# Kernel tuning notes

Hardware: AMD Instinct MI355X
Metric: run time of the kernel (lower is better)

The kernel has to match this reference:

```python
import jax, jax.numpy as jnp
import numpy as np
import math

N = 4096
D = 256


def _xavier(key, shape):
    fan_in, fan_out = shape[0], shape[1]
    std = math.sqrt(2.0 / (fan_in + fan_out))
    return jax.random.normal(key, shape, dtype=jnp.float32) * std


def setup_inputs() -> dict:
    key = jax.random.key(0)
    ks = jax.random.split(key, 12)
    return {
        "cur": jax.random.normal(ks[0], (N, D), dtype=jnp.float32),
        "pre": jax.random.normal(ks[1], (N, D), dtype=jnp.float32),
        # SpatialHyperedge params
        "r_proj_s": _xavier(ks[2], (D, D)),
        "incidence_s": _xavier(ks[3], (N, N - 1)),
        # TemporalHyperedge params
        "r_proj_t": _xavier(ks[4], (D, D)),
        "incidence_t": _xavier(ks[5], (N, N)),
        # HHNodeMP params
        "node_proj": _xavier(ks[6], (D, D)),
        "spa_edge_proj": _xavier(ks[7], (D, D)),
        "tmp_edge_proj": _xavier(ks[8], (D, D)),
        "theta_w": _xavier(ks[9], (D, D)),
        "theta_b": jnp.zeros((D,), dtype=jnp.float32),
    }


def _scatter_slave(vals):
    """Place [N, N-1] per-row slave values into a zero-diagonal [N, N] matrix.
    Row i's k-th slave is column k if k < i else k+1 (all j != i in order)."""
    n = vals.shape[0]
    k = jnp.arange(n - 1)[None, :]
    cols = k + (k >= jnp.arange(n)[:, None])  # [N, N-1] column indices
    rows = jnp.broadcast_to(jnp.arange(n)[:, None], (n, n - 1))
    return jnp.zeros((n, n), dtype=vals.dtype).at[rows.reshape(-1), cols.reshape(-1)].set(vals.reshape(-1))


def _fro(x):
    return jnp.sqrt(jnp.sum(x * x))


def reference(cur, pre, r_proj_s, incidence_s, r_proj_t, incidence_t,
              node_proj, spa_edge_proj, tmp_edge_proj, theta_w, theta_b):
    n, d = cur.shape
    inv_sqrt_d = 1.0 / math.sqrt(d)

    # ---- SpatialHyperedge ----
    Xd = jax.lax.stop_gradient(cur)
    master_s = Xd @ r_proj_s                                   # [N, D]
    M_s_full = _scatter_slave(incidence_s)                     # [N, N], zero diag
    neigh_recon_s = M_s_full @ Xd                              # == bmm over gathered slaves
    spatial_loss = (_fro(master_s - neigh_recon_s) * 0.2
                    + jnp.sum(jnp.abs(incidence_s))
                    + 0.001 * _fro(incidence_s))
    # clamp(min=0) then zero-out entries not strictly > 0  => relu-like
    clipped_s = jnp.where(incidence_s > 0.0, incidence_s, 0.0)
    incidence_all = _scatter_slave(clipped_s) + jnp.eye(n, dtype=cur.dtype)

    # ---- TemporalHyperedge ----
    cur_d = jax.lax.stop_gradient(cur)
    pre_d = jax.lax.stop_gradient(pre)
    master_t = cur_d @ r_proj_t
    neigh_recon_t = incidence_t @ pre_d
    temporal_loss = (_fro(master_t - neigh_recon_t) * 0.2
                     + jnp.sum(jnp.abs(incidence_t))
                     + 0.001 * _fro(incidence_t))
    incidence_t_clipped = jnp.maximum(incidence_t, 0.0)

    # ---- SpatialHyperedgeMP ----
    spa_edge_fea = incidence_all @ cur
    spa_deg = jnp.sum(incidence_all, axis=1, keepdims=True)
    spa_emb = spa_edge_fea / spa_deg                           # [N, D]

    # ---- TemporalHyperedgeMP ----
    tmp_edge_fea = incidence_t_clipped @ pre + cur
    tmp_deg = jnp.sum(incidence_t_clipped, axis=1, keepdims=True) + 1.0
    tmp_emb = tmp_edge_fea / tmp_deg                           # [N, D]

    # ---- HHNodeMP ----
    node_fea = cur @ node_proj
    spa_fea = spa_emb @ spa_edge_proj
    tmp_fea = tmp_emb @ tmp_edge_proj
    spa_attn = jnp.sum(spa_fea * node_fea, axis=1, keepdims=True) * inv_sqrt_d
    tmp_attn = jnp.sum(tmp_fea * node_fea, axis=1, keepdims=True) * inv_sqrt_d
    val = spa_attn * spa_fea + tmp_attn * tmp_fea
    node_emb = jax.nn.relu(val @ theta_w.T + theta_b)          # dropout = identity (eval)

    return node_emb, temporal_loss + spatial_loss
```

## Files before the change

kernel.cpp:

```cpp
#include <hip/hip_runtime.h>
#include <hip/hip_bf16.h>
#include <math.h>

#define NN 4096
#define DD 256

typedef __bf16 bf16x8 __attribute__((ext_vector_type(8)));
typedef short  short8 __attribute__((ext_vector_type(8)));
typedef float  f32x4  __attribute__((ext_vector_type(4)));

#define MFMA16(a, b, c) __builtin_amdgcn_mfma_f32_16x16x32_bf16((a), (b), (c), 0, 0, 0)

__device__ inline bf16x8 brelu(bf16x8 a) {
    short8 s = __builtin_bit_cast(short8, a);
    s = s & ~(s >> 15);
    return __builtin_bit_cast(bf16x8, s);
}

__device__ inline float wave_red(float v) {
#pragma unroll
    for (int o = 32; o > 0; o >>= 1) v += __shfl_down(v, o, 64);
    return v;
}

__device__ inline unsigned short bfbits(float f) {
    return __builtin_bit_cast(unsigned short, (__bf16)f);
}

__global__ __launch_bounds__(256) void k_prep(const float* __restrict__ cur,
                                              const float* __restrict__ pre,
                                              __bf16* __restrict__ cur_bf,
                                              __bf16* __restrict__ curT,
                                              __bf16* __restrict__ preT) {
    const int z = blockIdx.z;
    const int i0 = blockIdx.x * 64, d0 = blockIdx.y * 64;
    const float* src = z ? pre : cur;
    __bf16* dstT = z ? preT : curT;
    __shared__ unsigned short tile[64][72];
    const int t = threadIdx.x;
    const int r = t >> 2, c4 = (t & 3) * 16;
    const float* srow = src + (size_t)(i0 + r) * DD + d0 + c4;
    alignas(16) unsigned short loc[16];
#pragma unroll
    for (int e = 0; e < 4; ++e) {
        float4 v = ((const float4*)srow)[e];
        loc[e * 4 + 0] = bfbits(v.x);
        loc[e * 4 + 1] = bfbits(v.y);
        loc[e * 4 + 2] = bfbits(v.z);
        loc[e * 4 + 3] = bfbits(v.w);
    }
#pragma unroll
    for (int e = 0; e < 16; ++e) tile[r][c4 + e] = loc[e];
    if (z == 0) {
        __bf16* drow = cur_bf + (size_t)(i0 + r) * DD + d0 + c4;
        *(uint4*)drow = *(uint4*)&loc[0];
        *(uint4*)(drow + 8) = *(uint4*)&loc[8];
    }
    __syncthreads();
    alignas(16) unsigned short o[16];
#pragma unroll
    for (int e = 0; e < 16; ++e) o[e] = tile[c4 + e][r];
    __bf16* trow = dstT + (size_t)(d0 + r) * NN + i0 + c4;
    *(uint4*)trow = *(uint4*)&o[0];
    *(uint4*)(trow + 8) = *(uint4*)&o[8];
}

__global__ __launch_bounds__(256) void k_proj(
    const float* __restrict__ a0, const float* __restrict__ a1, const float* __restrict__ a2,
    const float* __restrict__ a3, const float* __restrict__ a4, const float* __restrict__ a5,
    __bf16* __restrict__ o0, __bf16* __restrict__ o1, __bf16* __restrict__ o2,
    __bf16* __restrict__ o3, __bf16* __restrict__ o4, __bf16* __restrict__ o5) {
    const int id = blockIdx.y, r = blockIdx.x, t = threadIdx.x;
    const float* src = id == 0 ? a0 : id == 1 ? a1 : id == 2 ? a2 : id == 3 ? a3 : id == 4 ? a4 : a5;
    __bf16* dst = id == 0 ? o0 : id == 1 ? o1 : id == 2 ? o2 : id == 3 ? o3 : id == 4 ? o4 : o5;
    float v = src[r * DD + t];
    if (id < 5) dst[t * DD + r] = (__bf16)v;
    else        dst[r * DD + t] = (__bf16)v;
}

__global__ __launch_bounds__(256) void k_conv(const float* __restrict__ incT, const float* __restrict__ incS,
                                              __bf16* __restrict__ Mt, __bf16* __restrict__ Ms,
                                              float* __restrict__ rsT, float* __restrict__ rsS,
                                              float* __restrict__ pAbsT, float* __restrict__ pSqT,
                                              float* __restrict__ pAbsS, float* __restrict__ pSqS) {
    const int i = blockIdx.x, t = threadIdx.x;
    __shared__ unsigned short row[NN];
    __shared__ float red[3][4];
    float rs = 0.f, as = 0.f, qs = 0.f;
    if (blockIdx.y == 0) {
        const float4* src = (const float4*)(incT + (size_t)i * NN);
        ushort4* dst = (ushort4*)(Mt + (size_t)i * NN);
#pragma unroll
        for (int e = 0; e < 4; ++e) {
            const int f = t + 256 * e;
            float4 v = src[f];
            float x[4] = {v.x, v.y, v.z, v.w};
            unsigned short o[4];
#pragma unroll
            for (int j = 0; j < 4; ++j) {
                float fv = x[j];
                as += fabsf(fv); qs += fv * fv; rs += fmaxf(fv, 0.f);
                o[j] = bfbits(fv);
            }
            dst[f] = make_ushort4(o[0], o[1], o[2], o[3]);
        }
        const int w = t >> 6, lane = t & 63;
        rs = wave_red(rs); as = wave_red(as); qs = wave_red(qs);
        if (lane == 0) { red[0][w] = rs; red[1][w] = as; red[2][w] = qs; }
        __syncthreads();
        if (t == 0) {
            rsT[i]   = red[0][0] + red[0][1] + red[0][2] + red[0][3];
            pAbsT[i] = red[1][0] + red[1][1] + red[1][2] + red[1][3];
            pSqT[i]  = red[2][0] + red[2][1] + red[2][2] + red[2][3];
        }
    } else {
        const float* srow = incS + (size_t)i * (NN - 1);
#pragma unroll
        for (int e = 0; e < 4; ++e) {
            const int f = t + 256 * e;
            float x[4] = {0.f, 0.f, 0.f, 0.f};
            if (f < 1023) __builtin_memcpy(x, srow + 4 * f, 16);
            else          __builtin_memcpy(x, srow + 4092, 12);
#pragma unroll
            for (int j = 0; j < 4; ++j) {
                const int k = 4 * f + j;
                float fv = x[j];
                as += fabsf(fv); qs += fv * fv; rs += fmaxf(fv, 0.f);
                if (k < NN - 1) row[k + (k >= i)] = bfbits(fv);
            }
        }
        if (t == 0) row[i] = 0;
        __syncthreads();
        uint4* dOut = (uint4*)(Ms + (size_t)i * NN);
        const uint4* sIn = (const uint4*)row;
        dOut[t] = sIn[t];
        dOut[t + 256] = sIn[t + 256];
        const int w = t >> 6, lane = t & 63;
        rs = wave_red(rs); as = wave_red(as); qs = wave_red(qs);
        if (lane == 0) { red[0][w] = rs; red[1][w] = as; red[2][w] = qs; }
        __syncthreads();
        if (t == 0) {
            rsS[i]   = red[0][0] + red[0][1] + red[0][2] + red[0][3];
            pAbsS[i] = red[1][0] + red[1][1] + red[1][2] + red[1][3];
            pSqS[i]  = red[2][0] + red[2][1] + red[2][2] + red[2][3];
        }
    }
}

__global__ __launch_bounds__(256) void k_big(const __bf16* __restrict__ Mt, const __bf16* __restrict__ Ms,
                                             const __bf16* __restrict__ preT, const __bf16* __restrict__ curT,
                                             const float* __restrict__ negMt, const float* __restrict__ negMs,
                                             const float* __restrict__ cur,
                                             float* __restrict__ feaT, float* __restrict__ feaS,
                                             float* __restrict__ pDiff) {
    const int z = blockIdx.y;
    const __bf16* A  = z ? Ms : Mt;
    const __bf16* BT = z ? curT : preT;
    const float* negM = z ? negMs : negMt;
    float* fea = z ? feaS : feaT;
    const int m0 = blockIdx.x * 32;
    __shared__ __bf16 As[2][32][64];
    __shared__ float sred[4];
    const int t = threadIdx.x, w = t >> 6, lane = t & 63, quad = lane >> 4, l16 = lane & 15;
    const int rsw = l16 & 7;
    const int srow = t >> 3, sc8 = t & 7;
    const int swz = (sc8 ^ (srow & 7)) * 8;
    const __bf16* gA = A + (size_t)(m0 + srow) * NN + sc8 * 8;
    const int nb = w * 64;
    const __bf16* gB[4];
#pragma unroll
    for (int nf = 0; nf < 4; ++nf)
        gB[nf] = BT + (size_t)(nb + nf * 16 + l16) * NN + quad * 8;

    f32x4 accR[2][4], accL[2][4];
#pragma unroll
    for (int mi = 0; mi < 2; ++mi)
#pragma unroll
        for (int nf = 0; nf < 4; ++nf) { accR[mi][nf] = (f32x4)0.f; accL[mi][nf] = (f32x4)0.f; }

    bf16x8 b[2][2][4];
    uint4 preA;
    {
        uint4 a0 = *(const uint4*)gA; gA += 64;
        *(uint4*)&As[0][srow][swz] = a0;
        preA = *(const uint4*)gA; gA += 64;
#pragma unroll
        for (int ks = 0; ks < 2; ++ks)
#pragma unroll
            for (int nf = 0; nf < 4; ++nf)
                b[0][ks][nf] = *(const bf16x8*)(gB[nf] + ks * 32);
        __syncthreads();
    }
#pragma unroll 2
    for (int kt = 0; kt < 64; ++kt) {
        const int cb = kt & 1;
        if (kt < 63) *(uint4*)&As[cb ^ 1][srow][swz] = preA;
        if (kt < 62) { preA = *(const uint4*)gA; gA += 64; }
        if (kt < 63) {
#pragma unroll
            for (int ks = 0; ks < 2; ++ks)
#pragma unroll
                for (int nf = 0; nf < 4; ++nf)
                    b[cb ^ 1][ks][nf] = *(const bf16x8*)(gB[nf] + (kt + 1) * 64 + ks * 32);
        }
        bf16x8 a[2][2];
#pragma unroll
        for (int ks = 0; ks < 2; ++ks) {
            const int col = ((ks * 4 + quad) ^ rsw) * 8;
#pragma unroll
            for (int mi = 0; mi < 2; ++mi)
                a[ks][mi] = *(const bf16x8*)&As[cb][mi * 16 + l16][col];
        }
#pragma unroll
        for (int ks = 0; ks < 2; ++ks)
#pragma unroll
            for (int mi = 0; mi < 2; ++mi) {
                bf16x8 ar = brelu(a[ks][mi]);
#pragma unroll
                for (int nf = 0; nf < 4; ++nf) {
                    accR[mi][nf] = MFMA16(a[ks][mi], b[cb][ks][nf], accR[mi][nf]);
                    accL[mi][nf] = MFMA16(ar, b[cb][ks][nf], accL[mi][nf]);
                }
            }
        __syncthreads();
    }
    float sumd = 0.f;
#pragma unroll
    for (int mi = 0; mi < 2; ++mi)
#pragma unroll
        for (int nf = 0; nf < 4; ++nf)
#pragma unroll
            for (int r = 0; r < 4; ++r) {
                int gr = m0 + mi * 16 + quad * 4 + r;
                int gc = nb + nf * 16 + l16;
                size_t idx = (size_t)gr * DD + gc;
                float diff = accR[mi][nf][r] + negM[idx];
                sumd += diff * diff;
                fea[idx] = accL[mi][nf][r] + cur[idx];
            }
    sumd = wave_red(sumd);
    if (lane == 0) sred[w] = sumd;
    __syncthreads();
    if (t == 0) pDiff[z * 128 + blockIdx.x] = sred[0] + sred[1] + sred[2] + sred[3];
}

template <int DUAL>
__device__ inline void mfma_step(const __bf16 (&As)[64][72], const __bf16 (&Bs)[64][72],
                                 int wr, int wc, int quad, int l16,
                                 f32x4 (&accR)[2][2], f32x4 (&accL)[2][2]) {
#pragma unroll
    for (int ks = 0; ks < 2; ++ks) {
        const int kc = ks * 32 + quad * 8;
        bf16x8 a0 = *(const bf16x8*)&As[wr * 32 + l16][kc];
        bf16x8 a1 = *(const bf16x8*)&As[wr * 32 + 16 + l16][kc];
        bf16x8 b0 = *(const bf16x8*)&Bs[wc * 32 + l16][kc];
        bf16x8 b1 = *(const bf16x8*)&Bs[wc * 32 + 16 + l16][kc];
        accR[0][0] = MFMA16(a0, b0, accR[0][0]);
        accR[0][1] = MFMA16(a0, b1, accR[0][1]);
        accR[1][0] = MFMA16(a1, b0, accR[1][0]);
        accR[1][1] = MFMA16(a1, b1, accR[1][1]);
        if (DUAL) {
            bf16x8 a0r = brelu(a0), a1r = brelu(a1);
            accL[0][0] = MFMA16(a0r, b0, accL[0][0]);
            accL[0][1] = MFMA16(a0r, b1, accL[0][1]);
            accL[1][0] = MFMA16(a1r, b0, accL[1][0]);
            accL[1][1] = MFMA16(a1r, b1, accL[1][1]);
        }
    }
}

__global__ __launch_bounds__(256) void k_small3(const __bf16* __restrict__ cur_bf,
                                                const __bf16* __restrict__ pTs, const __bf16* __restrict__ pTt,
                                                const __bf16* __restrict__ pTn,
                                                float* __restrict__ negMs, float* __restrict__ negMt,
                                                float* __restrict__ nodeFea) {
    const int z = blockIdx.z;
    const __bf16* BT = z == 0 ? pTs : (z == 1 ? pTt : pTn);
    const int n0 = blockIdx.x * 64, m0 = blockIdx.y * 64;
    __shared__ __bf16 As[64][72], Bs[64][72];
    f32x4 accR[2][2];
#pragma unroll
    for (int i = 0; i < 2; ++i)
#pragma unroll
        for (int j = 0; j < 2; ++j) accR[i][j] = (f32x4)0.f;
    const int t = threadIdx.x, w = t >> 6, lane = t & 63, quad = lane >> 4, l16 = lane & 15;
    const int wr = w >> 1, wc = w & 1;
    const int sr = t >> 2, sc = (t & 3) * 16;
    const __bf16* gA = cur_bf + (size_t)(m0 + sr) * DD + sc;
    const __bf16* gB = BT + (size_t)(n0 + sr) * DD + sc;
    for (int kt = 0; kt < DD / 64; ++kt) {
        uint4 av0 = *(const uint4*)(gA);
        uint4 av1 = *(const uint4*)(gA + 8);
        uint4 bv0 = *(const uint4*)(gB);
        uint4 bv1 = *(const uint4*)(gB + 8);
        __syncthreads();
        *(uint4*)&As[sr][sc] = av0; *(uint4*)&As[sr][sc + 8] = av1;
        *(uint4*)&Bs[sr][sc] = bv0; *(uint4*)&Bs[sr][sc + 8] = bv1;
        __syncthreads();
        mfma_step<0>(As, Bs, wr, wc, quad, l16, accR, accR);
        gA += 64; gB += 64;
    }
#pragma unroll
    for (int mi = 0; mi < 2; ++mi)
#pragma unroll
        for (int ni = 0; ni < 2; ++ni)
#pragma unroll
            for (int r = 0; r < 4; ++r) {
                int gr = m0 + wr * 32 + mi * 16 + quad * 4 + r;
                int gc = n0 + wc * 32 + ni * 16 + l16;
                size_t idx = (size_t)gr * DD + gc;
                float v = accR[mi][ni][r];
                if (z == 0) negMs[idx] = -v;
                else if (z == 1) negMt[idx] = -v;
                else nodeFea[idx] = v;
            }
}

__global__ __launch_bounds__(256) void k_fea(const float* __restrict__ feaS, const float* __restrict__ feaT,
                                             const float* __restrict__ rsS, const float* __restrict__ rsT,
                                             const __bf16* __restrict__ pTspa, const __bf16* __restrict__ pTtmp,
                                             float* __restrict__ spaF, float* __restrict__ tmpF) {
    const int z = blockIdx.z;
    const float* fea = z ? feaT : feaS;
    const float* rs = z ? rsT : rsS;
    const __bf16* BT = z ? pTtmp : pTspa;
    float* outF = z ? tmpF : spaF;
    const int n0 = blockIdx.x * 64, m0 = blockIdx.y * 64;
    __shared__ __bf16 As[64][72], Bs[64][72];
    f32x4 accR[2][2];
#pragma unroll
    for (int i = 0; i < 2; ++i)
#pragma unroll
        for (int j = 0; j < 2; ++j) accR[i][j] = (f32x4)0.f;
    const int t = threadIdx.x, w = t >> 6, lane = t & 63, quad = lane >> 4, l16 = lane & 15;
    const int wr = w >> 1, wc = w & 1;
    const int sr = t >> 2, sc = (t & 3) * 16;
    const float inv = 1.f / (rs[m0 + sr] + 1.f);
    const float* gA = fea + (size_t)(m0 + sr) * DD + sc;
    const __bf16* gB = BT + (size_t)(n0 + sr) * DD + sc;
    for (int kt = 0; kt < DD / 64; ++kt) {
        __bf16 tmp[16];
#pragma unroll
        for (int e4 = 0; e4 < 4; ++e4) {
            float4 v = ((const float4*)gA)[e4];
            tmp[e4 * 4 + 0] = (__bf16)(v.x * inv);
            tmp[e4 * 4 + 1] = (__bf16)(v.y * inv);
            tmp[e4 * 4 + 2] = (__bf16)(v.z * inv);
            tmp[e4 * 4 + 3] = (__bf16)(v.w * inv);
        }
        uint4 bv0 = *(const uint4*)(gB);
        uint4 bv1 = *(const uint4*)(gB + 8);
        __syncthreads();
        *(uint4*)&As[sr][sc] = *(uint4*)&tmp[0]; *(uint4*)&As[sr][sc + 8] = *(uint4*)&tmp[8];
        *(uint4*)&Bs[sr][sc] = bv0; *(uint4*)&Bs[sr][sc + 8] = bv1;
        __syncthreads();
        mfma_step<0>(As, Bs, wr, wc, quad, l16, accR, accR);
        gA += 64; gB += 64;
    }
#pragma unroll
    for (int mi = 0; mi < 2; ++mi)
#pragma unroll
        for (int ni = 0; ni < 2; ++ni)
#pragma unroll
            for (int r = 0; r < 4; ++r) {
                int gr = m0 + wr * 32 + mi * 16 + quad * 4 + r;
                int gc = n0 + wc * 32 + ni * 16 + l16;
                outF[(size_t)gr * DD + gc] = accR[mi][ni][r];
            }
}

__global__ __launch_bounds__(256) void k_attn(const float* __restrict__ spaF, const float* __restrict__ tmpF,
                                              const float* __restrict__ nodeF,
                                              float* __restrict__ spaA, float* __restrict__ tmpA) {
    const int t = threadIdx.x, w = t >> 6, lane = t & 63;
    const int i = blockIdx.x * 4 + w;
    const float4* sf = (const float4*)(spaF + (size_t)i * DD);
    const float4* tf = (const float4*)(tmpF + (size_t)i * DD);
    const float4* nf = (const float4*)(nodeF + (size_t)i * DD);
    float4 s = sf[lane], p = tf[lane], n = nf[lane];
    float ds = s.x * n.x + s.y * n.y + s.z * n.z + s.w * n.w;
    float dt = p.x * n.x + p.y * n.y + p.z * n.z + p.w * n.w;
    ds = wave_red(ds); dt = wave_red(dt);
    if (lane == 0) { spaA[i] = ds * 0.0625f; tmpA[i] = dt * 0.0625f; }
}

__global__ __launch_bounds__(256) void k_final(const float* __restrict__ spaF, const float* __restrict__ tmpF,
                                               const float* __restrict__ spaA, const float* __restrict__ tmpA,
                                               const __bf16* __restrict__ thetaBf, const float* __restrict__ thetaB,
                                               float* __restrict__ out) {
    const int n0 = blockIdx.x * 64, m0 = blockIdx.y * 64;
    __shared__ __bf16 As[64][72], Bs[64][72];
    f32x4 accR[2][2];
#pragma unroll
    for (int i = 0; i < 2; ++i)
#pragma unroll
        for (int j = 0; j < 2; ++j) accR[i][j] = (f32x4)0.f;
    const int t = threadIdx.x, w = t >> 6, lane = t & 63, quad = lane >> 4, l16 = lane & 15;
    const int wr = w >> 1, wc = w & 1;
    const int sr = t >> 2, sc = (t & 3) * 16;
    const float sa = spaA[m0 + sr], ta = tmpA[m0 + sr];
    const float* gS = spaF + (size_t)(m0 + sr) * DD + sc;
    const float* gT = tmpF + (size_t)(m0 + sr) * DD + sc;
    const __bf16* gB = thetaBf + (size_t)(n0 + sr) * DD + sc;
    for (int kt = 0; kt < DD / 64; ++kt) {
        __bf16 tmp[16];
#pragma unroll
        for (int e4 = 0; e4 < 4; ++e4) {
            float4 vs = ((const float4*)gS)[e4];
            float4 vt = ((const float4*)gT)[e4];
            tmp[e4 * 4 + 0] = (__bf16)(sa * vs.x + ta * vt.x);
            tmp[e4 * 4 + 1] = (__bf16)(sa * vs.y + ta * vt.y);
            tmp[e4 * 4 + 2] = (__bf16)(sa * vs.z + ta * vt.z);
            tmp[e4 * 4 + 3] = (__bf16)(sa * vs.w + ta * vt.w);
        }
        uint4 bv0 = *(const uint4*)(gB);
        uint4 bv1 = *(const uint4*)(gB + 8);
        __syncthreads();
        *(uint4*)&As[sr][sc] = *(uint4*)&tmp[0]; *(uint4*)&As[sr][sc + 8] = *(uint4*)&tmp[8];
        *(uint4*)&Bs[sr][sc] = bv0; *(uint4*)&Bs[sr][sc + 8] = bv1;
        __syncthreads();
        mfma_step<0>(As, Bs, wr, wc, quad, l16, accR, accR);
        gS += 64; gT += 64; gB += 64;
    }
#pragma unroll
    for (int mi = 0; mi < 2; ++mi)
#pragma unroll
        for (int ni = 0; ni < 2; ++ni)
#pragma unroll
            for (int r = 0; r < 4; ++r) {
                int gr = m0 + wr * 32 + mi * 16 + quad * 4 + r;
                int gc = n0 + wc * 32 + ni * 16 + l16;
                float v = accR[mi][ni][r] + thetaB[gc];
                out[(size_t)gr * DD + gc] = fmaxf(v, 0.f);
            }
}

__global__ __launch_bounds__(256) void k_loss(const float* __restrict__ pAbsT, const float* __restrict__ pSqT,
                                              const float* __restrict__ pAbsS, const float* __restrict__ pSqS,
                                              const float* __restrict__ pDiff,
                                              float* __restrict__ out) {
    const int t = threadIdx.x;
    float aT = 0.f, qT = 0.f, aS = 0.f, qS = 0.f;
#pragma unroll
    for (int j = 0; j < 16; ++j) {
        const int i = t + 256 * j;
        aT += pAbsT[i]; qT += pSqT[i]; aS += pAbsS[i]; qS += pSqS[i];
    }
    float pd = pDiff[t];
    float dT = t < 128 ? pd : 0.f;
    float dS = t < 128 ? 0.f : pd;
    aT = wave_red(aT); qT = wave_red(qT); aS = wave_red(aS); qS = wave_red(qS);
    dT = wave_red(dT); dS = wave_red(dS);
    __shared__ float red[6][4];
    const int w = t >> 6, lane = t & 63;
    if (lane == 0) { red[0][w] = aT; red[1][w] = qT; red[2][w] = aS; red[3][w] = qS; red[4][w] = dT; red[5][w] = dS; }
    __syncthreads();
    if (t == 0) {
        float s[6];
#pragma unroll
        for (int k = 0; k < 6; ++k) s[k] = red[k][0] + red[k][1] + red[k][2] + red[k][3];
        float l = s[0] + 0.001f * sqrtf(s[1]) + 0.2f * sqrtf(s[4])
                + s[2] + 0.001f * sqrtf(s[3]) + 0.2f * sqrtf(s[5]);
        out[(size_t)NN * DD] = l;
    }
}

extern "C" void kernel_launch(void* const* d_in, const int* in_sizes, int n_in,
                              void* d_out, int out_size, void* d_ws, size_t ws_size,
                              hipStream_t stream) {
    (void)in_sizes; (void)n_in; (void)out_size; (void)ws_size;
    const float* cur      = (const float*)d_in[0];
    const float* pre      = (const float*)d_in[1];
    const float* r_proj_s = (const float*)d_in[2];
    const float* inc_s    = (const float*)d_in[3];
    const float* r_proj_t = (const float*)d_in[4];
    const float* inc_t    = (const float*)d_in[5];
    const float* node_pj  = (const float*)d_in[6];
    const float* spa_pj   = (const float*)d_in[7];
    const float* tmp_pj   = (const float*)d_in[8];
    const float* theta_w  = (const float*)d_in[9];
    const float* theta_b  = (const float*)d_in[10];
    float* out = (float*)d_out;

    char* p = (char*)d_ws;
    auto alloc = [&](size_t bytes) -> void* {
        void* r = (void*)p;
        p += (bytes + 255) & ~(size_t)255;
        return r;
    };
    __bf16* Mt      = (__bf16*)alloc((size_t)NN * NN * 2);
    __bf16* Ms      = (__bf16*)alloc((size_t)NN * NN * 2);
    __bf16* cur_bf  = (__bf16*)alloc((size_t)NN * DD * 2);
    __bf16* curT    = (__bf16*)alloc((size_t)NN * DD * 2);
    __bf16* preT    = (__bf16*)alloc((size_t)NN * DD * 2);
    __bf16* pTs     = (__bf16*)alloc((size_t)DD * DD * 2);
    __bf16* pTt     = (__bf16*)alloc((size_t)DD * DD * 2);
    __bf16* pTn     = (__bf16*)alloc((size_t)DD * DD * 2);
    __bf16* pTspa   = (__bf16*)alloc((size_t)DD * DD * 2);
    __bf16* pTtmp   = (__bf16*)alloc((size_t)DD * DD * 2);
    __bf16* thetaBf = (__bf16*)alloc((size_t)DD * DD * 2);
    float* negMs    = (float*)alloc((size_t)NN * DD * 4);
    float* negMt    = (float*)alloc((size_t)NN * DD * 4);
    float* nodeFea  = (float*)alloc((size_t)NN * DD * 4);
    float* feaS     = (float*)alloc((size_t)NN * DD * 4);
    float* feaT     = (float*)alloc((size_t)NN * DD * 4);
    float* spaF     = (float*)alloc((size_t)NN * DD * 4);
    float* tmpF     = (float*)alloc((size_t)NN * DD * 4);
    float* rsS      = (float*)alloc((size_t)NN * 4);
    float* rsT      = (float*)alloc((size_t)NN * 4);
    float* spaA     = (float*)alloc((size_t)NN * 4);
    float* tmpA     = (float*)alloc((size_t)NN * 4);
    float* pAbsT    = (float*)alloc((size_t)NN * 4);
    float* pSqT     = (float*)alloc((size_t)NN * 4);
    float* pAbsS    = (float*)alloc((size_t)NN * 4);
    float* pSqS     = (float*)alloc((size_t)NN * 4);
    float* pDiff    = (float*)alloc(256 * 4);

    k_prep<<<dim3(NN / 64, DD / 64, 2), 256, 0, stream>>>(cur, pre, cur_bf, curT, preT);
    k_proj<<<dim3(DD, 6), 256, 0, stream>>>(r_proj_s, r_proj_t, node_pj, spa_pj, tmp_pj, theta_w,
                                            pTs, pTt, pTn, pTspa, pTtmp, thetaBf);
    k_conv<<<dim3(NN, 2), 256, 0, stream>>>(inc_t, inc_s, Mt, Ms, rsT, rsS, pAbsT, pSqT, pAbsS, pSqS);
    k_small3<<<dim3(4, 64, 3), 256, 0, stream>>>(cur_bf, pTs, pTt, pTn, negMs, negMt, nodeFea);
    k_big<<<dim3(128, 2), 256, 0, stream>>>(Mt, Ms, preT, curT, negMt, negMs, cur, feaT, feaS, pDiff);
    k_fea<<<dim3(4, 64, 2), 256, 0, stream>>>(feaS, feaT, rsS, rsT, pTspa, pTtmp, spaF, tmpF);
    k_attn<<<NN / 4, 256, 0, stream>>>(spaF, tmpF, nodeFea, spaA, tmpA);
    k_final<<<dim3(4, 64), 256, 0, stream>>>(spaF, tmpF, spaA, tmpA, thetaBf, theta_b, out);
    k_loss<<<1, 256, 0, stream>>>(pAbsT, pSqT, pAbsS, pSqS, pDiff, out);
}
```

Baseline: 292.5 us.

## Merge preprocessing kernels into one launch and widen big GEMM to 512 threads

Folds the transpose/convert, weight-projection conversion, incidence conversion, and small projection GEMMs into one block-indexed kernel. The small GEMMs now convert fp32 inputs on the fly instead of reading pre-converted bf16 copies. This drops several launches and intermediate buffers. The main incidence GEMM is restructured to 512 threads with a 128-wide K tile, double-buffered swizzled LDS, and register prefetch, aiming for better latency hiding over the large 4096x4096 reads. The risk is that the fused kernel's strided fp32 weight reads and heavier per-block register use could offset the gains.

```diff
diff --git a/kernel.cpp b/kernel.cpp
--- a/kernel.cpp
+++ b/kernel.cpp
@@ -27,127 +27,213 @@
     return __builtin_bit_cast(unsigned short, (__bf16)f);
 }
 
-__global__ __launch_bounds__(256) void k_prep(const float* __restrict__ cur,
-                                              const float* __restrict__ pre,
-                                              __bf16* __restrict__ cur_bf,
-                                              __bf16* __restrict__ curT,
-                                              __bf16* __restrict__ preT) {
-    const int z = blockIdx.z;
-    const int i0 = blockIdx.x * 64, d0 = blockIdx.y * 64;
-    const float* src = z ? pre : cur;
-    __bf16* dstT = z ? preT : curT;
-    __shared__ unsigned short tile[64][72];
-    const int t = threadIdx.x;
-    const int r = t >> 2, c4 = (t & 3) * 16;
-    const float* srow = src + (size_t)(i0 + r) * DD + d0 + c4;
-    alignas(16) unsigned short loc[16];
-#pragma unroll
-    for (int e = 0; e < 4; ++e) {
-        float4 v = ((const float4*)srow)[e];
-        loc[e * 4 + 0] = bfbits(v.x);
-        loc[e * 4 + 1] = bfbits(v.y);
-        loc[e * 4 + 2] = bfbits(v.z);
-        loc[e * 4 + 3] = bfbits(v.w);
-    }
-#pragma unroll
-    for (int e = 0; e < 16; ++e) tile[r][c4 + e] = loc[e];
-    if (z == 0) {
-        __bf16* drow = cur_bf + (size_t)(i0 + r) * DD + d0 + c4;
-        *(uint4*)drow = *(uint4*)&loc[0];
-        *(uint4*)(drow + 8) = *(uint4*)&loc[8];
-    }
-    __syncthreads();
-    alignas(16) unsigned short o[16];
-#pragma unroll
-    for (int e = 0; e < 16; ++e) o[e] = tile[c4 + e][r];
-    __bf16* trow = dstT + (size_t)(d0 + r) * NN + i0 + c4;
-    *(uint4*)trow = *(uint4*)&o[0];
-    *(uint4*)(trow + 8) = *(uint4*)&o[8];
-}
-
-__global__ __launch_bounds__(256) void k_proj(
-    const float* __restrict__ a0, const float* __restrict__ a1, const float* __restrict__ a2,
-    const float* __restrict__ a3, const float* __restrict__ a4, const float* __restrict__ a5,
-    __bf16* __restrict__ o0, __bf16* __restrict__ o1, __bf16* __restrict__ o2,
-    __bf16* __restrict__ o3, __bf16* __restrict__ o4, __bf16* __restrict__ o5) {
-    const int id = blockIdx.y, r = blockIdx.x, t = threadIdx.x;
-    const float* src = id == 0 ? a0 : id == 1 ? a1 : id == 2 ? a2 : id == 3 ? a3 : id == 4 ? a4 : a5;
-    __bf16* dst = id == 0 ? o0 : id == 1 ? o1 : id == 2 ? o2 : id == 3 ? o3 : id == 4 ? o4 : o5;
-    float v = src[r * DD + t];
-    if (id < 5) dst[t * DD + r] = (__bf16)v;
-    else        dst[r * DD + t] = (__bf16)v;
-}
-
-__global__ __launch_bounds__(256) void k_conv(const float* __restrict__ incT, const float* __restrict__ incS,
-                                              __bf16* __restrict__ Mt, __bf16* __restrict__ Ms,
-                                              float* __restrict__ rsT, float* __restrict__ rsS,
-                                              float* __restrict__ pAbsT, float* __restrict__ pSqT,
-                                              float* __restrict__ pAbsS, float* __restrict__ pSqS) {
-    const int i = blockIdx.x, t = threadIdx.x;
-    __shared__ unsigned short row[NN];
-    __shared__ float red[3][4];
-    float rs = 0.f, as = 0.f, qs = 0.f;
-    if (blockIdx.y == 0) {
-        const float4* src = (const float4*)(incT + (size_t)i * NN);
-        ushort4* dst = (ushort4*)(Mt + (size_t)i * NN);
+__global__ __launch_bounds__(256) void k_pre(
+    const float* __restrict__ cur, const float* __restrict__ pre,
+    const float* __restrict__ r_proj_s, const float* __restrict__ inc_s,
+    const float* __restrict__ r_proj_t, const float* __restrict__ inc_t,
+    const float* __restrict__ node_pj, const float* __restrict__ spa_pj,
+    const float* __restrict__ tmp_pj, const float* __restrict__ theta_w,
+    __bf16* __restrict__ Mt, __bf16* __restrict__ Ms,
+    __bf16* __restrict__ curT, __bf16* __restrict__ preT,
+    __bf16* __restrict__ pTspa, __bf16* __restrict__ pTtmp, __bf16* __restrict__ thetaBf,
+    float* __restrict__ negMs, float* __restrict__ negMt, float* __restrict__ nodeFea,
+    float* __restrict__ rsT, float* __restrict__ rsS,
+    float* __restrict__ pAbsT, float* __restrict__ pSqT,
+    float* __restrict__ pAbsS, float* __restrict__ pSqS)
+{
+    __shared__ __align__(16) char sm[18496];
+    const int bx = blockIdx.x, t = threadIdx.x;
+
+    if (bx < 8192) {
+        float (*red)[4] = (float(*)[4])(sm + 8192 + 64);
+        float rs = 0.f, as = 0.f, qs = 0.f;
+        const int w = t >> 6, lane = t & 63;
+        if (bx < 4096) {
+            const int i = bx;
+            const float4* src = (const float4*)(inc_t + (size_t)i * NN);
+            ushort4* dst = (ushort4*)(Mt + (size_t)i * NN);
+#pragma unroll
+            for (int e = 0; e < 4; ++e) {
+                const int f = t + 256 * e;
+                float4 v = src[f];
+                float x[4] = {v.x, v.y, v.z, v.w};
+                unsigned short o[4];
+#pragma unroll
+                for (int j = 0; j < 4; ++j) {
+                    float fv = x[j];
+                    as += fabsf(fv); qs += fv * fv; rs += fmaxf(fv, 0.f);
+                    o[j] = bfbits(fv);
+                }
+                dst[f] = make_ushort4(o[0], o[1], o[2], o[3]);
+            }
+            rs = wave_red(rs); as = wave_red(as); qs = wave_red(qs);
+            if (lane == 0) { red[0][w] = rs; red[1][w] = as; red[2][w] = qs; }
+            __syncthreads();
+            if (t == 0) {
+                rsT[i]   = red[0][0] + red[0][1] + red[0][2] + red[0][3];
+                pAbsT[i] = red[1][0] + red[1][1] + red[1][2] + red[1][3];
+                pSqT[i]  = red[2][0] + red[2][1] + red[2][2] + red[2][3];
+            }
+        } else {
+            const int i = bx - 4096;
+            unsigned short* row = (unsigned short*)sm;
+            const float* srow = inc_s + (size_t)i * (NN - 1);
+#pragma unroll
+            for (int e = 0; e < 4; ++e) {
+                const int f = t + 256 * e;
+                float x[4] = {0.f, 0.f, 0.f, 0.f};
+                if (f < 1023) __builtin_memcpy(x, srow + 4 * f, 16);
+                else          __builtin_memcpy(x, srow + 4092, 12);
+#pragma unroll
+                for (int j = 0; j < 4; ++j) {
+                    const int k = 4 * f + j;
+                    float fv = x[j];
+                    as += fabsf(fv); qs += fv * fv; rs += fmaxf(fv, 0.f);
+                    if (k < NN - 1) row[k + (k >= i)] = bfbits(fv);
+                }
+            }
+            if (t == 0) row[i] = 0;
+            __syncthreads();
+            uint4* dOut = (uint4*)(Ms + (size_t)i * NN);
+            const uint4* sIn = (const uint4*)row;
+            dOut[t] = sIn[t];
+            dOut[t + 256] = sIn[t + 256];
+            rs = wave_red(rs); as = wave_red(as); qs = wave_red(qs);
+            if (lane == 0) { red[0][w] = rs; red[1][w] = as; red[2][w] = qs; }
+            __syncthreads();
+            if (t == 0) {
+                rsS[i]   = red[0][0] + red[0][1] + red[0][2] + red[0][3];
+                pAbsS[i] = red[1][0] + red[1][1] + red[1][2] + red[1][3];
+                pSqS[i]  = red[2][0] + red[2][1] + red[2][2] + red[2][3];
+            }
+        }
+    } else if (bx < 8704) {
+        const int idx = bx - 8192;
+        const int z = idx >> 8, yt = (idx >> 6) & 3, xt = idx & 63;
+        const int i0 = xt * 64, d0 = yt * 64;
+        const float* src = z ? pre : cur;
+        __bf16* dstT = z ? preT : curT;
+        unsigned short (*tile)[72] = (unsigned short(*)[72])sm;
+        const int r = t >> 2, c4 = (t & 3) * 16;
+        const float* srow = src + (size_t)(i0 + r) * DD + d0 + c4;
+        alignas(16) unsigned short loc[16];
 #pragma unroll
         for (int e = 0; e < 4; ++e) {
-            const int f = t + 256 * e;
-            float4 v = src[f];
-            float x[4] = {v.x, v.y, v.z, v.w};
-            unsigned short o[4];
-#pragma unroll
-            for (int j = 0; j < 4; ++j) {
-                float fv = x[j];
-                as += fabsf(fv); qs += fv * fv; rs += fmaxf(fv, 0.f);
-                o[j] = bfbits(fv);
-            }
-            dst[f] = make_ushort4(o[0], o[1], o[2], o[3]);
-        }
-        const int w = t >> 6, lane = t & 63;
-        rs = wave_red(rs); as = wave_red(as); qs = wave_red(qs);
-        if (lane == 0) { red[0][w] = rs; red[1][w] = as; red[2][w] = qs; }
+            float4 v = ((const float4*)srow)[e];
+            loc[e * 4 + 0] = bfbits(v.x); loc[e * 4 + 1] = bfbits(v.y);
+            loc[e * 4 + 2] = bfbits(v.z); loc[e * 4 + 3] = bfbits(v.w);
+        }
+#pragma unroll
+        for (int e = 0; e < 16; ++e) tile[r][c4 + e] = loc[e];
         __syncthreads();
-        if (t == 0) {
-            rsT[i]   = red[0][0] + red[0][1] + red[0][2] + red[0][3];
-            pAbsT[i] = red[1][0] + red[1][1] + red[1][2] + red[1][3];
-            pSqT[i]  = red[2][0] + red[2][1] + red[2][2] + red[2][3];
+        alignas(16) unsigned short o[16];
+#pragma unroll
+        for (int e = 0; e < 16; ++e) o[e] = tile[c4 + e][r];
+        __bf16* trow = dstT + (size_t)(d0 + r) * NN + i0 + c4;
+        *(uint4*)trow = *(uint4*)&o[0];
+        *(uint4*)(trow + 8) = *(uint4*)&o[8];
+    } else if (bx < 8752) {
+        const int idx = bx - 8704;
+        const int m = idx >> 4, tt = idx & 15;
+        const int k0 = (tt >> 2) * 64, n0 = (tt & 3) * 64;
+        const int r = t >> 2, c4 = (t & 3) * 16;
+        if (m < 2) {
+            const float* src = m == 0 ? spa_pj : tmp_pj;
+            __bf16* dst = m == 0 ? pTspa : pTtmp;
+            unsigned short (*tile)[72] = (unsigned short(*)[72])sm;
+            const float* srow = src + (size_t)(k0 + r) * DD + n0 + c4;
+            alignas(16) unsigned short loc[16];
+#pragma unroll
+            for (int e = 0; e < 4; ++e) {
+                float4 v = ((const float4*)srow)[e];
+                loc[e * 4 + 0] = bfbits(v.x); loc[e * 4 + 1] = bfbits(v.y);
+                loc[e * 4 + 2] = bfbits(v.z); loc[e * 4 + 3] = bfbits(v.w);
+            }
+#pragma unroll
+            for (int e = 0; e < 16; ++e) tile[r][c4 + e] = loc[e];
+            __syncthreads();
+            alignas(16) unsigned short o[16];
+#pragma unroll
+            for (int e = 0; e < 16; ++e) o[e] = tile[c4 + e][r];
+            __bf16* trow = dst + (size_t)(n0 + r) * DD + k0 + c4;
+            *(uint4*)trow = *(uint4*)&o[0];
+            *(uint4*)(trow + 8) = *(uint4*)&o[8];
+        } else {
+            const float* srow = theta_w + (size_t)(k0 + r) * DD + n0 + c4;
+            alignas(16) unsigned short loc[16];
+#pragma unroll
+            for (int e = 0; e < 4; ++e) {
+                float4 v = ((const float4*)srow)[e];
+                loc[e * 4 + 0] = bfbits(v.x); loc[e * 4 + 1] = bfbits(v.y);
+                loc[e * 4 + 2] = bfbits(v.z); loc[e * 4 + 3] = bfbits(v.w);
+            }
+            __bf16* drow = thetaBf + (size_t)(k0 + r) * DD + n0 + c4;
+            *(uint4*)drow = *(uint4*)&loc[0];
+            *(uint4*)(drow + 8) = *(uint4*)&loc[8];
         }
     } else {
-        const float* srow = incS + (size_t)i * (NN - 1);
-#pragma unroll
-        for (int e = 0; e < 4; ++e) {
-            const int f = t + 256 * e;
-            float x[4] = {0.f, 0.f, 0.f, 0.f};
-            if (f < 1023) __builtin_memcpy(x, srow + 4 * f, 16);
-            else          __builtin_memcpy(x, srow + 4092, 12);
-#pragma unroll
-            for (int j = 0; j < 4; ++j) {
-                const int k = 4 * f + j;
-                float fv = x[j];
-                as += fabsf(fv); qs += fv * fv; rs += fmaxf(fv, 0.f);
-                if (k < NN - 1) row[k + (k >= i)] = bfbits(fv);
-            }
-        }
-        if (t == 0) row[i] = 0;
-        __syncthreads();
-        uint4* dOut = (uint4*)(Ms + (size_t)i * NN);
-        const uint4* sIn = (const uint4*)row;
-        dOut[t] = sIn[t];
-        dOut[t + 256] = sIn[t + 256];
-        const int w = t >> 6, lane = t & 63;
-        rs = wave_red(rs); as = wave_red(as); qs = wave_red(qs);
-        if (lane == 0) { red[0][w] = rs; red[1][w] = as; red[2][w] = qs; }
-        __syncthreads();
-        if (t == 0) {
-            rsS[i]   = red[0][0] + red[0][1] + red[0][2] + red[0][3];
-            pAbsS[i] = red[1][0] + red[1][1] + red[1][2] + red[1][3];
-            pSqS[i]  = red[2][0] + red[2][1] + red[2][2] + red[2][3];
-        }
-    }
-}
-
-__global__ __launch_bounds__(256) void k_big(const __bf16* __restrict__ Mt, const __bf16* __restrict__ Ms,
+        const int idx = bx - 8752;
+        const int z = idx >> 8, r2 = idx & 255;
+        const int n0 = (r2 & 3) * 64, m0 = (r2 >> 2) * 64;
+        const float* srcB = z == 0 ? r_proj_s : (z == 1 ? r_proj_t : node_pj);
+        __bf16 (*As)[72] = (__bf16(*)[72])sm;
+        __bf16 (*Bs)[72] = (__bf16(*)[72])(sm + 9232);
+        f32x4 acc[2][2];
+#pragma unroll
+        for (int i = 0; i < 2; ++i)
+#pragma unroll
+            for (int j = 0; j < 2; ++j) acc[i][j] = (f32x4)0.f;
+        const int w = t >> 6, lane = t & 63, quad = lane >> 4, l16 = lane & 15;
+        const int wr = w >> 1, wc = w & 1;
+        const int sr = t >> 2, sc = (t & 3) * 16;
+        for (int kt = 0; kt < 4; ++kt) {
+            const int k0 = kt * 64;
+            alignas(16) __bf16 av[16], bv[16];
+            const float* arow = cur + (size_t)(m0 + sr) * DD + k0 + sc;
+#pragma unroll
+            for (int e4 = 0; e4 < 4; ++e4) {
+                float4 v = ((const float4*)arow)[e4];
+                av[e4 * 4 + 0] = (__bf16)v.x; av[e4 * 4 + 1] = (__bf16)v.y;
+                av[e4 * 4 + 2] = (__bf16)v.z; av[e4 * 4 + 3] = (__bf16)v.w;
+            }
+#pragma unroll
+            for (int e = 0; e < 16; ++e)
+                bv[e] = (__bf16)srcB[(size_t)(k0 + sc + e) * DD + n0 + sr];
+            __syncthreads();
+            *(uint4*)&As[sr][sc] = *(uint4*)&av[0]; *(uint4*)&As[sr][sc + 8] = *(uint4*)&av[8];
+            *(uint4*)&Bs[sr][sc] = *(uint4*)&bv[0]; *(uint4*)&Bs[sr][sc + 8] = *(uint4*)&bv[8];
+            __syncthreads();
+#pragma unroll
+            for (int ks = 0; ks < 2; ++ks) {
+                const int kc = ks * 32 + quad * 8;
+                bf16x8 a0 = *(const bf16x8*)&As[wr * 32 + l16][kc];
+                bf16x8 a1 = *(const bf16x8*)&As[wr * 32 + 16 + l16][kc];
+                bf16x8 b0 = *(const bf16x8*)&Bs[wc * 32 + l16][kc];
+                bf16x8 b1 = *(const bf16x8*)&Bs[wc * 32 + 16 + l16][kc];
+                acc[0][0] = MFMA16(a0, b0, acc[0][0]);
+                acc[0][1] = MFMA16(a0, b1, acc[0][1]);
+                acc[1][0] = MFMA16(a1, b0, acc[1][0]);
+                acc[1][1] = MFMA16(a1, b1, acc[1][1]);
+            }
+        }
+#pragma unroll
+        for (int mi = 0; mi < 2; ++mi)
+#pragma unroll
+            for (int ni = 0; ni < 2; ++ni)
+#pragma unroll
+                for (int r = 0; r < 4; ++r) {
+                    int gr = m0 + wr * 32 + mi * 16 + quad * 4 + r;
+                    int gc = n0 + wc * 32 + ni * 16 + l16;
+                    size_t o = (size_t)gr * DD + gc;
+                    float v = acc[mi][ni][r];
+                    if (z == 0) negMs[o] = -v;
+                    else if (z == 1) negMt[o] = -v;
+                    else nodeFea[o] = v;
+                }
+    }
+}
+
+__global__ __launch_bounds__(512) void k_big(const __bf16* __restrict__ Mt, const __bf16* __restrict__ Ms,
                                              const __bf16* __restrict__ preT, const __bf16* __restrict__ curT,
                                              const float* __restrict__ negMt, const float* __restrict__ negMs,
                                              const float* __restrict__ cur,
@@ -159,95 +245,87 @@
     const float* negM = z ? negMs : negMt;
     float* fea = z ? feaS : feaT;
     const int m0 = blockIdx.x * 32;
-    __shared__ __bf16 As[2][32][64];
-    __shared__ float sred[4];
+    __shared__ __bf16 As[2][32 * 128];
+    __shared__ float sred[8];
     const int t = threadIdx.x, w = t >> 6, lane = t & 63, quad = lane >> 4, l16 = lane & 15;
-    const int rsw = l16 & 7;
-    const int srow = t >> 3, sc8 = t & 7;
-    const int swz = (sc8 ^ (srow & 7)) * 8;
-    const __bf16* gA = A + (size_t)(m0 + srow) * NN + sc8 * 8;
-    const int nb = w * 64;
-    const __bf16* gB[4];
+    const int wr = w >> 2, wc = w & 3;
+    const int srow = t >> 4, c8 = t & 15;
+    const int scb = c8 >> 1, shalf = c8 & 1;
+    const int sofs = srow * 128 + ((scb ^ (srow & 7)) << 4) + shalf * 8;
+    const __bf16* gA = A + (size_t)(m0 + srow) * NN + c8 * 8;
+    const int nb = wc * 64;
+    const __bf16* gB0 = BT + (size_t)(nb + l16) * NN + quad * 8;
+    const int arow = wr * 16 + l16;
+    const int abase = arow * 128;
+    const int asw = arow & 7;
+
+    f32x4 accR[4], accL[4];
+#pragma unroll
+    for (int nf = 0; nf < 4; ++nf) { accR[nf] = (f32x4)0.f; accL[nf] = (f32x4)0.f; }
+
+    uint4 pA = *(const uint4*)gA; gA += 128;
+    *(uint4*)&As[0][sofs] = pA;
+    pA = *(const uint4*)gA; gA += 128;
+    __syncthreads();
+
+    for (int kt = 0; kt < 32; ++kt) {
+        const int cb = kt & 1;
+        if (kt < 31) {
+            *(uint4*)&As[cb ^ 1][sofs] = pA;
+            if (kt < 30) { pA = *(const uint4*)gA; gA += 128; }
+        }
+        const size_t kgl = (size_t)kt * 128;
+        bf16x8 b[4], bn[4];
+#pragma unroll
+        for (int nf = 0; nf < 4; ++nf)
+            b[nf] = *(const bf16x8*)(gB0 + (size_t)nf * 16 * NN + kgl);
+#pragma unroll
+        for (int ks = 0; ks < 4; ++ks) {
+            if (ks < 3) {
+#pragma unroll
+                for (int nf = 0; nf < 4; ++nf)
+                    bn[nf] = *(const bf16x8*)(gB0 + (size_t)nf * 16 * NN + kgl + (ks + 1) * 32);
+            }
+            const int acb = ks * 2 + (quad >> 1);
+            bf16x8 a = *(const bf16x8*)&As[cb][abase + ((acb ^ asw) << 4) + (quad & 1) * 8];
+            bf16x8 ar = brelu(a);
+#pragma unroll
+            for (int nf = 0; nf < 4; ++nf) {
+                accR[nf] = MFMA16(a, b[nf], accR[nf]);
+                accL[nf] = MFMA16(ar, b[nf], accL[nf]);
+            }
+            if (ks < 3) {
+#pragma unroll
+                for (int nf = 0; nf < 4; ++nf) b[nf] = bn[nf];
+            }
+        }
+        __syncthreads();
+    }
+    float sumd = 0.f;
 #pragma unroll
     for (int nf = 0; nf < 4; ++nf)
-        gB[nf] = BT + (size_t)(nb + nf * 16 + l16) * NN + quad * 8;
-
-    f32x4 accR[2][4], accL[2][4];
-#pragma unroll
-    for (int mi = 0; mi < 2; ++mi)
-#pragma unroll
-        for (int nf = 0; nf < 4; ++nf) { accR[mi][nf] = (f32x4)0.f; accL[mi][nf] = (f32x4)0.f; }
-
-    bf16x8 b[2][2][4];
-    uint4 preA;
-    {
-        uint4 a0 = *(const uint4*)gA; gA += 64;
-        *(uint4*)&As[0][srow][swz] = a0;
-        preA = *(const uint4*)gA; gA += 64;
-#pragma unroll
-        for (int ks = 0; ks < 2; ++ks)
-#pragma unroll
-            for (int nf = 0; nf < 4; ++nf)
-                b[0][ks][nf] = *(const bf16x8*)(gB[nf] + ks * 32);
-        __syncthreads();
-    }
-#pragma unroll 2
-    for (int kt = 0; kt < 64; ++kt) {
-        const int cb = kt & 1;
-        if (kt < 63) *(uint4*)&As[cb ^ 1][srow][swz] = preA;
-        if (kt < 62) { preA = *(const uint4*)gA; gA += 64; }
-        if (kt < 63) {
-#pragma unroll
-            for (int ks = 0; ks < 2; ++ks)
-#pragma unroll
-                for (int nf = 0; nf < 4; ++nf)
-                    b[cb ^ 1][ks][nf] = *(const bf16x8*)(gB[nf] + (kt + 1) * 64 + ks * 32);
-        }
-        bf16x8 a[2][2];
-#pragma unroll
-        for (int ks = 0; ks < 2; ++ks) {
-            const int col = ((ks * 4 + quad) ^ rsw) * 8;
-#pragma unroll
-            for (int mi = 0; mi < 2; ++mi)
-                a[ks][mi] = *(const bf16x8*)&As[cb][mi * 16 + l16][col];
-        }
-#pragma unroll
-        for (int ks = 0; ks < 2; ++ks)
-#pragma unroll
-            for (int mi = 0; mi < 2; ++mi) {
-                bf16x8 ar = brelu(a[ks][mi]);
-#pragma unroll
-                for (int nf = 0; nf < 4; ++nf) {
-                    accR[mi][nf] = MFMA16(a[ks][mi], b[cb][ks][nf], accR[mi][nf]);
-                    accL[mi][nf] = MFMA16(ar, b[cb][ks][nf], accL[mi][nf]);
-                }
-            }
-        __syncthreads();
-    }
-    float sumd = 0.f;
-#pragma unroll
-    for (int mi = 0; mi < 2; ++mi)
-#pragma unroll
-        for (int nf = 0; nf < 4; ++nf)
-#pragma unroll
-            for (int r = 0; r < 4; ++r) {
-                int gr = m0 + mi * 16 + quad * 4 + r;
-                int gc = nb + nf * 16 + l16;
-                size_t idx = (size_t)gr * DD + gc;
-                float diff = accR[mi][nf][r] + negM[idx];
-                sumd += diff * diff;
-                fea[idx] = accL[mi][nf][r] + cur[idx];
-            }
+#pragma unroll
+        for (int r = 0; r < 4; ++r) {
+            int gr = m0 + wr * 16 + quad * 4 + r;
+            int gc = nb + nf * 16 + l16;
+            size_t idx = (size_t)gr * DD + gc;
+            float diff = accR[nf][r] + negM[idx];
+            sumd += diff * diff;
+            fea[idx] = accL[nf][r] + cur[idx];
+        }
     sumd = wave_red(sumd);
     if (lane == 0) sred[w] = sumd;
     __syncthreads();
-    if (t == 0) pDiff[z * 128 + blockIdx.x] = sred[0] + sred[1] + sred[2] + sred[3];
-}
-
-template <int DUAL>
-__device__ inline void mfma_step(const __bf16 (&As)[64][72], const __bf16 (&Bs)[64][72],
-                                 int wr, int wc, int quad, int l16,
-                                 f32x4 (&accR)[2][2], f32x4 (&accL)[2][2]) {
+    if (t == 0) {
+        float s = 0.f;
+#pragma unroll
+        for (int i = 0; i < 8; ++i) s += sred[i];
+        pDiff[z * 128 + blockIdx.x] = s;
+    }
+}
+
+__device__ inline void mfma_step0(const __bf16 (*As)[72], const __bf16 (*Bs)[72],
+                                  int wr, int wc, int quad, int l16, f32x4 (&acc)[2][2]) {
 #pragma unroll
     for (int ks = 0; ks < 2; ++ks) {
         const int kc = ks * 32 + quad * 8;
@@ -255,65 +333,11 @@
         bf16x8 a1 = *(const bf16x8*)&As[wr * 32 + 16 + l16][kc];
         bf16x8 b0 = *(const bf16x8*)&Bs[wc * 32 + l16][kc];
         bf16x8 b1 = *(const bf16x8*)&Bs[wc * 32 + 16 + l16][kc];
-        accR[0][0] = MFMA16(a0, b0, accR[0][0]);
-        accR[0][1] = MFMA16(a0, b1, accR[0][1]);
-        accR[1][0] = MFMA16(a1, b0, accR[1][0]);
-        accR[1][1] = MFMA16(a1, b1, accR[1][1]);
-        if (DUAL) {
-            bf16x8 a0r = brelu(a0), a1r = brelu(a1);
-            accL[0][0] = MFMA16(a0r, b0, accL[0][0]);
-            accL[0][1] = MFMA16(a0r, b1, accL[0][1]);
-            accL[1][0] = MFMA16(a1r, b0, accL[1][0]);
-            accL[1][1] = MFMA16(a1r, b1, accL[1][1]);
-        }
-    }
-}
-
-__global__ __launch_bounds__(256) void k_small3(const __bf16* __restrict__ cur_bf,
-                                                const __bf16* __restrict__ pTs, const __bf16* __restrict__ pTt,
-                                                const __bf16* __restrict__ pTn,
-                                                float* __restrict__ negMs, float* __restrict__ negMt,
-                                                float* __restrict__ nodeFea) {
-    const int z = blockIdx.z;
-    const __bf16* BT = z == 0 ? pTs : (z == 1 ? pTt : pTn);
-    const int n0 = blockIdx.x * 64, m0 = blockIdx.y * 64;
-    __shared__ __bf16 As[64][72], Bs[64][72];
-    f32x4 accR[2][2];
-#pragma unroll
-    for (int i = 0; i < 2; ++i)
-#pragma unroll
-        for (int j = 0; j < 2; ++j) accR[i][j] = (f32x4)0.f;
-    const int t = threadIdx.x, w = t >> 6, lane = t & 63, quad = lane >> 4, l16 = lane & 15;
-    const int wr = w >> 1, wc = w & 1;
-    const int sr = t >> 2, sc = (t & 3) * 16;
-    const __bf16* gA = cur_bf + (size_t)(m0 + sr) * DD + sc;
-    const __bf16* gB = BT + (size_t)(n0 + sr) * DD + sc;
-    for (int kt = 0; kt < DD / 64; ++kt) {
-        uint4 av0 = *(const uint4*)(gA);
-        uint4 av1 = *(const uint4*)(gA + 8);
-        uint4 bv0 = *(const uint4*)(gB);
-        uint4 bv1 = *(const uint4*)(gB + 8);
-        __syncthreads();
-        *(uint4*)&As[sr][sc] = av0; *(uint4*)&As[sr][sc + 8] = av1;
-        *(uint4*)&Bs[sr][sc] = bv0; *(uint4*)&Bs[sr][sc + 8] = bv1;
-        __syncthreads();
-        mfma_step<0>(As, Bs, wr, wc, quad, l16, accR, accR);
-        gA += 64; gB += 64;
-    }
-#pragma unroll
-    for (int mi = 0; mi < 2; ++mi)
-#pragma unroll
-        for (int ni = 0; ni < 2; ++ni)
-#pragma unroll
-            for (int r = 0; r < 4; ++r) {
-                int gr = m0 + wr * 32 + mi * 16 + quad * 4 + r;
-                int gc = n0 + wc * 32 + ni * 16 + l16;
-                size_t idx = (size_t)gr * DD + gc;
-                float v = accR[mi][ni][r];
-                if (z == 0) negMs[idx] = -v;
-                else if (z == 1) negMt[idx] = -v;
-                else nodeFea[idx] = v;
-            }
+        acc[0][0] = MFMA16(a0, b0, acc[0][0]);
+        acc[0][1] = MFMA16(a0, b1, acc[0][1]);
+        acc[1][0] = MFMA16(a1, b0, acc[1][0]);
+        acc[1][1] = MFMA16(a1, b1, acc[1][1]);
+    }
 }
 
 __global__ __launch_bounds__(256) void k_fea(const float* __restrict__ feaS, const float* __restrict__ feaT,
@@ -327,11 +351,11 @@
     float* outF = z ? tmpF : spaF;
     const int n0 = blockIdx.x * 64, m0 = blockIdx.y * 64;
     __shared__ __bf16 As[64][72], Bs[64][72];
-    f32x4 accR[2][2];
+    f32x4 acc[2][2];
 #pragma unroll
     for (int i = 0; i < 2; ++i)
 #pragma unroll
-        for (int j = 0; j < 2; ++j) accR[i][j] = (f32x4)0.f;
+        for (int j = 0; j < 2; ++j) acc[i][j] = (f32x4)0.f;
     const int t = threadIdx.x, w = t >> 6, lane = t & 63, quad = lane >> 4, l16 = lane & 15;
     const int wr = w >> 1, wc = w & 1;
     const int sr = t >> 2, sc = (t & 3) * 16;
@@ -354,7 +378,7 @@
         *(uint4*)&As[sr][sc] = *(uint4*)&tmp[0]; *(uint4*)&As[sr][sc + 8] = *(uint4*)&tmp[8];
         *(uint4*)&Bs[sr][sc] = bv0; *(uint4*)&Bs[sr][sc + 8] = bv1;
         __syncthreads();
-        mfma_step<0>(As, Bs, wr, wc, quad, l16, accR, accR);
+        mfma_step0(As, Bs, wr, wc, quad, l16, acc);
         gA += 64; gB += 64;
     }
 #pragma unroll
@@ -365,7 +389,7 @@
             for (int r = 0; r < 4; ++r) {
                 int gr = m0 + wr * 32 + mi * 16 + quad * 4 + r;
                 int gc = n0 + wc * 32 + ni * 16 + l16;
-                outF[(size_t)gr * DD + gc] = accR[mi][ni][r];
+                outF[(size_t)gr * DD + gc] = acc[mi][ni][r];
             }
 }
 
@@ -390,11 +414,11 @@
                                                float* __restrict__ out) {
     const int n0 = blockIdx.x * 64, m0 = blockIdx.y * 64;
     __shared__ __bf16 As[64][72], Bs[64][72];
-    f32x4 accR[2][2];
+    f32x4 acc[2][2];
 #pragma unroll
     for (int i = 0; i < 2; ++i)
 #pragma unroll
-        for (int j = 0; j < 2; ++j) accR[i][j] = (f32x4)0.f;
+        for (int j = 0; j < 2; ++j) acc[i][j] = (f32x4)0.f;
     const int t = threadIdx.x, w = t >> 6, lane = t & 63, quad = lane >> 4, l16 = lane & 15;
     const int wr = w >> 1, wc = w & 1;
     const int sr = t >> 2, sc = (t & 3) * 16;
@@ -419,7 +443,7 @@
         *(uint4*)&As[sr][sc] = *(uint4*)&tmp[0]; *(uint4*)&As[sr][sc + 8] = *(uint4*)&tmp[8];
         *(uint4*)&Bs[sr][sc] = bv0; *(uint4*)&Bs[sr][sc + 8] = bv1;
         __syncthreads();
-        mfma_step<0>(As, Bs, wr, wc, quad, l16, accR, accR);
+        mfma_step0(As, Bs, wr, wc, quad, l16, acc);
         gS += 64; gT += 64; gB += 64;
     }
 #pragma unroll
@@ -430,7 +454,7 @@
             for (int r = 0; r < 4; ++r) {
                 int gr = m0 + wr * 32 + mi * 16 + quad * 4 + r;
                 int gc = n0 + wc * 32 + ni * 16 + l16;
-                float v = accR[mi][ni][r] + thetaB[gc];
+                float v = acc[mi][ni][r] + thetaB[gc];
                 out[(size_t)gr * DD + gc] = fmaxf(v, 0.f);
             }
 }
@@ -490,12 +514,8 @@
     };
     __bf16* Mt      = (__bf16*)alloc((size_t)NN * NN * 2);
     __bf16* Ms      = (__bf16*)alloc((size_t)NN * NN * 2);
-    __bf16* cur_bf  = (__bf16*)alloc((size_t)NN * DD * 2);
     __bf16* curT    = (__bf16*)alloc((size_t)NN * DD * 2);
     __bf16* preT    = (__bf16*)alloc((size_t)NN * DD * 2);
-    __bf16* pTs     = (__bf16*)alloc((size_t)DD * DD * 2);
-    __bf16* pTt     = (__bf16*)alloc((size_t)DD * DD * 2);
-    __bf16* pTn     = (__bf16*)alloc((size_t)DD * DD * 2);
     __bf16* pTspa   = (__bf16*)alloc((size_t)DD * DD * 2);
     __bf16* pTtmp   = (__bf16*)alloc((size_t)DD * DD * 2);
     __bf16* thetaBf = (__bf16*)alloc((size_t)DD * DD * 2);
@@ -516,12 +536,12 @@
     float* pSqS     = (float*)alloc((size_t)NN * 4);
     float* pDiff    = (float*)alloc(256 * 4);
 
-    k_prep<<<dim3(NN / 64, DD / 64, 2), 256, 0, stream>>>(cur, pre, cur_bf, curT, preT);
-    k_proj<<<dim3(DD, 6), 256, 0, stream>>>(r_proj_s, r_proj_t, node_pj, spa_pj, tmp_pj, theta_w,
-                                            pTs, pTt, pTn, pTspa, pTtmp, thetaBf);
-    k_conv<<<dim3(NN, 2), 256, 0, stream>>>(inc_t, inc_s, Mt, Ms, rsT, rsS, pAbsT, pSqT, pAbsS, pSqS);
-    k_small3<<<dim3(4, 64, 3), 256, 0, stream>>>(cur_bf, pTs, pTt, pTn, negMs, negMt, nodeFea);
-    k_big<<<dim3(128, 2), 256, 0, stream>>>(Mt, Ms, preT, curT, negMt, negMs, cur, feaT, feaS, pDiff);
+    k_pre<<<9520, 256, 0, stream>>>(cur, pre, r_proj_s, inc_s, r_proj_t, inc_t,
+                                    node_pj, spa_pj, tmp_pj, theta_w,
+                                    Mt, Ms, curT, preT, pTspa, pTtmp, thetaBf,
+                                    negMs, negMt, nodeFea,
+                                    rsT, rsS, pAbsT, pSqT, pAbsS, pSqS);
+    k_big<<<dim3(128, 2), 512, 0, stream>>>(Mt, Ms, preT, curT, negMt, negMs, cur, feaT, feaS, pDiff);
     k_fea<<<dim3(4, 64, 2), 256, 0, stream>>>(feaS, feaT, rsS, rsT, pTspa, pTtmp, spaF, tmpF);
     k_attn<<<NN / 4, 256, 0, stream>>>(spaF, tmpF, nodeFea, spaA, tmpA);
     k_final<<<dim3(4, 64), 256, 0, stream>>>(spaF, tmpF, spaA, tmpA, thetaBf, theta_b, out);
```

New measurement: 337.7 us. 15.5% more time.
